# Kernel optimization log

Measured on AMD Instinct MI355X. Metric: run time of the kernel, lower is better.

## Reference

```python
import jax, jax.numpy as jnp
import numpy as np

H, KVH, D = 32, 8, 128
HID = H * D
OP = H * D + 2 * KVH * D
T = 2048
LAYER_IDX = 8
LAMBDA_INIT = float(0.8 - 0.6 * np.exp(-0.3 * LAYER_IDX))
EPS = 1e-5


def setup_inputs() -> dict:
    key = jax.random.key(0)
    ks = jax.random.split(key, 10)
    s = 0.02
    return {
        "hidden_states": jax.random.normal(ks[0], (T, HID), jnp.float32),
        "wqkv_w": jax.random.normal(ks[1], (OP, HID), jnp.float32) * s,
        "wqkv_b": jax.random.normal(ks[2], (OP,), jnp.float32) * s,
        "lambda_q1": jax.random.normal(ks[3], (D,), jnp.float32) * 0.1,
        "lambda_k1": jax.random.normal(ks[4], (D,), jnp.float32) * 0.1,
        "lambda_q2": jax.random.normal(ks[5], (D,), jnp.float32) * 0.1,
        "lambda_k2": jax.random.normal(ks[6], (D,), jnp.float32) * 0.1,
        "subln_w": jnp.ones((2 * D,), jnp.float32),
        "out_w": jax.random.normal(ks[7], (HID, HID), jnp.float32) * s,
        "out_b": jax.random.normal(ks[8], (HID,), jnp.float32) * s,
    }


def reference(hidden_states, wqkv_w, wqkv_b, lambda_q1, lambda_k1,
              lambda_q2, lambda_k2, subln_w, out_w, out_b):
    t = hidden_states.shape[0]
    scale = D ** -0.5

    qkv = hidden_states @ wqkv_w.T + wqkv_b                     # [T, OP]
    q, k, v = jnp.split(qkv, [H * D, H * D + KVH * D], axis=-1)

    # pair-wise head split: consecutive heads form (pair, component) groups
    q = q.reshape(t, H // 2, 2, D)                              # [T, Hp, 2, D]
    k = k.reshape(t, KVH // 2, 2, D)                            # [T, KVHp, 2, D]
    v = v.reshape(t, KVH // 2, 2 * D)                           # [T, KVHp, 2D]

    rep = H // KVH  # GQA: query pair p -> kv pair p // rep
    k = jnp.repeat(k, rep, axis=1)                              # [T, Hp, 2, D]
    v = jnp.repeat(v, rep, axis=1)                              # [T, Hp, 2D]

    lam = (jnp.exp(jnp.dot(lambda_q1, lambda_k1))
           - jnp.exp(jnp.dot(lambda_q2, lambda_k2)) + LAMBDA_INIT)

    causal = jnp.tril(jnp.ones((t, t), bool))
    scores = jnp.einsum('qhcd,khcd->hcqk', q, k) * scale        # [Hp, 2, T, T]
    scores = jnp.where(causal, scores, -jnp.inf)
    probs = jax.nn.softmax(scores, axis=-1)
    attn = probs[:, 0] - lam * probs[:, 1]                      # [Hp, T, T]

    out = jnp.einsum('hqk,khd->qhd', attn, v)                   # [T, Hp, 2D]

    # per-head RMSNorm over 2D, scaled by (1 - lambda_init)
    rms = jax.lax.rsqrt(jnp.mean(out * out, axis=-1, keepdims=True) + EPS)
    out = out * rms * subln_w * (1.0 - LAMBDA_INIT)

    out = out.reshape(t, H * D)
    return out @ out_w.T + out_b
```

## Files before the change

### kernel.cpp

```cpp
#include <hip/hip_runtime.h>

#define TTOK 2048
#define HIDN 4096
#define OPD  6144
#define DH   128
#define VD   256
#define KOFF 4096
#define VOFF 5120

typedef short  s16x8 __attribute__((ext_vector_type(8)));
typedef unsigned short u16x8 __attribute__((ext_vector_type(8)));
typedef float  fx4   __attribute__((ext_vector_type(4)));

constexpr float LAM_INIT = 0.7455692280263534f;
constexpr float OML      = 1.0f - LAM_INIT;
constexpr float QKSCALE  = 0.08838834764831845f;
constexpr float RESCALE_THR = 8.0f;

__device__ __forceinline__ unsigned short f2bf(float f) {
  unsigned int u = __builtin_bit_cast(unsigned int, f);
  u += 0x7fffu + ((u >> 16) & 1u);
  return (unsigned short)(u >> 16);
}

__device__ __forceinline__ void g2l16(const void* gsrc, void* ldst) {
  __builtin_amdgcn_global_load_lds(
      (const __attribute__((address_space(1))) unsigned int*)gsrc,
      (__attribute__((address_space(3))) unsigned int*)ldst, 16, 0, 0);
}

__global__ __launch_bounds__(256)
void cvt3(const float* __restrict__ s0, unsigned short* __restrict__ d0, int nb0,
          const float* __restrict__ s1, unsigned short* __restrict__ d1, int nb1,
          const float* __restrict__ s2, unsigned short* __restrict__ d2)
{
  const int b = blockIdx.x;
  const float* s; unsigned short* d; int base;
  if (b < nb0)            { s = s0; d = d0; base = b << 11; }
  else if (b < nb0 + nb1) { s = s1; d = d1; base = (b - nb0) << 11; }
  else                    { s = s2; d = d2; base = (b - nb0 - nb1) << 11; }
  const int i = base + (int)threadIdx.x * 8;
  const float4 a0 = *(const float4*)(s + i);
  const float4 a1 = *(const float4*)(s + i + 4);
  u16x8 v;
  v[0]=f2bf(a0.x); v[1]=f2bf(a0.y); v[2]=f2bf(a0.z); v[3]=f2bf(a0.w);
  v[4]=f2bf(a1.x); v[5]=f2bf(a1.y); v[6]=f2bf(a1.z); v[7]=f2bf(a1.w);
  *(u16x8*)(d + i) = v;
}

template<int MW, bool QKVOUT, bool OUTBF16>
__global__ __launch_bounds__(512, 2)
void gemm_8ph(const unsigned short* __restrict__ A, const unsigned short* __restrict__ B,
              const float* __restrict__ bias, void* __restrict__ Cp,
              unsigned short* __restrict__ ctt, int K, int lda, int ldb, int ldc)
{
  constexpr int BM  = MW * 32;
  constexpr int ALD = BM / 64;
  __shared__ __align__(16) unsigned short As[2][BM * 64];
  __shared__ __align__(16) unsigned short Bs[2][256 * 64];

  const int tid  = threadIdx.x;
  const int lane = tid & 63, wid = tid >> 6;
  const int wm = wid >> 2, wn = wid & 3;
  const int m0 = blockIdx.y * BM, n0 = blockIdx.x * 256;
  const int l15 = lane & 15, lg = lane >> 4;

  const int srow = tid >> 3;
  const int scol = ((tid & 7) ^ ((tid >> 3) & 7)) << 3;
  const int rsw = (l15 & 7) << 3;
  const int ck0 = (lg * 8) ^ rsw;
  const int ck1 = (32 + lg * 8) ^ rsw;
  const int arow = wm * (MW * 16) + l15;
  const int brow = wn * 64 + l15;

  auto stageA = [&](int kt, int buf) {
    #pragma unroll
    for (int it = 0; it < ALD; ++it)
      g2l16(A + (size_t)(m0 + it * 64 + srow) * lda + kt + scol,
            &As[buf][(it * 512 + tid) * 8]);
  };
  auto stageB = [&](int kt, int buf, int h) {
    #pragma unroll
    for (int it = h * 2; it < h * 2 + 2; ++it)
      g2l16(B + (size_t)(n0 + it * 64 + srow) * ldb + kt + scol,
            &Bs[buf][(it * 512 + tid) * 8]);
  };

  fx4 acc[MW][4] = {};

  const int nk = K >> 6;
  stageA(0, 0); stageB(0, 0, 0); stageB(0, 0, 1);
  asm volatile("s_waitcnt vmcnt(0)" ::: "memory");
  __builtin_amdgcn_s_barrier();

  for (int t = 0; t < nk; ++t) {
    const unsigned short* as = As[t & 1];
    const unsigned short* bs = Bs[t & 1];
    const int kt1 = (t + 1) << 6;
    const int nb  = (t + 1) & 1;
    const bool pre = (t + 1) < nk;
    s16x8 af[MW], bf[4];

    #pragma unroll
    for (int mi = 0; mi < MW; ++mi)
      af[mi] = *(const s16x8*)&as[(arow + mi * 16) * 64 + ck0];
    bf[0] = *(const s16x8*)&bs[(brow +  0) * 64 + ck0];
    bf[1] = *(const s16x8*)&bs[(brow + 16) * 64 + ck0];
    if (pre) { stageA(kt1, nb); stageB(kt1, nb, 0); }
    __builtin_amdgcn_s_barrier();
    asm volatile("s_waitcnt lgkmcnt(0)" ::: "memory");
    __builtin_amdgcn_sched_barrier(0);
    __builtin_amdgcn_s_setprio(1);
    #pragma unroll
    for (int mi = 0; mi < MW; ++mi) {
      acc[mi][0] = __builtin_amdgcn_mfma_f32_16x16x32_bf16(af[mi], bf[0], acc[mi][0], 0, 0, 0);
      acc[mi][1] = __builtin_amdgcn_mfma_f32_16x16x32_bf16(af[mi], bf[1], acc[mi][1], 0, 0, 0);
    }
    __builtin_amdgcn_s_setprio(0);
    __builtin_amdgcn_s_barrier();

    bf[2] = *(const s16x8*)&bs[(brow + 32) * 64 + ck0];
    bf[3] = *(const s16x8*)&bs[(brow + 48) * 64 + ck0];
    if (pre) stageB(kt1, nb, 1);
    __builtin_amdgcn_s_barrier();
    asm volatile("s_waitcnt lgkmcnt(0)" ::: "memory");
    __builtin_amdgcn_sched_barrier(0);
    __builtin_amdgcn_s_setprio(1);
    #pragma unroll
    for (int mi = 0; mi < MW; ++mi) {
      acc[mi][2] = __builtin_amdgcn_mfma_f32_16x16x32_bf16(af[mi], bf[2], acc[mi][2], 0, 0, 0);
      acc[mi][3] = __builtin_amdgcn_mfma_f32_16x16x32_bf16(af[mi], bf[3], acc[mi][3], 0, 0, 0);
    }
    __builtin_amdgcn_s_setprio(0);
    __builtin_amdgcn_s_barrier();

    #pragma unroll
    for (int mi = 0; mi < MW; ++mi)
      af[mi] = *(const s16x8*)&as[(arow + mi * 16) * 64 + ck1];
    bf[0] = *(const s16x8*)&bs[(brow +  0) * 64 + ck1];
    bf[1] = *(const s16x8*)&bs[(brow + 16) * 64 + ck1];
    __builtin_amdgcn_s_barrier();
    asm volatile("s_waitcnt lgkmcnt(0)" ::: "memory");
    __builtin_amdgcn_sched_barrier(0);
    __builtin_amdgcn_s_setprio(1);
    #pragma unroll
    for (int mi = 0; mi < MW; ++mi) {
      acc[mi][0] = __builtin_amdgcn_mfma_f32_16x16x32_bf16(af[mi], bf[0], acc[mi][0], 0, 0, 0);
      acc[mi][1] = __builtin_amdgcn_mfma_f32_16x16x32_bf16(af[mi], bf[1], acc[mi][1], 0, 0, 0);
    }
    __builtin_amdgcn_s_setprio(0);
    __builtin_amdgcn_s_barrier();

    bf[2] = *(const s16x8*)&bs[(brow + 32) * 64 + ck1];
    bf[3] = *(const s16x8*)&bs[(brow + 48) * 64 + ck1];
    __builtin_amdgcn_s_barrier();
    asm volatile("s_waitcnt lgkmcnt(0)" ::: "memory");
    __builtin_amdgcn_sched_barrier(0);
    __builtin_amdgcn_s_setprio(1);
    #pragma unroll
    for (int mi = 0; mi < MW; ++mi) {
      acc[mi][2] = __builtin_amdgcn_mfma_f32_16x16x32_bf16(af[mi], bf[2], acc[mi][2], 0, 0, 0);
      acc[mi][3] = __builtin_amdgcn_mfma_f32_16x16x32_bf16(af[mi], bf[3], acc[mi][3], 0, 0, 0);
    }
    __builtin_amdgcn_s_setprio(0);
    if (pre) asm volatile("s_waitcnt vmcnt(0)" ::: "memory");
    __builtin_amdgcn_s_barrier();
  }

  const int r0 = m0 + wm * (MW * 16);
  const int c0 = n0 + wn * 64;
  if (QKVOUT && n0 >= VOFF) {
    #pragma unroll
    for (int mi = 0; mi < MW; ++mi)
      #pragma unroll
      for (int ni = 0; ni < 4; ++ni) {
        const int col = c0 + ni * 16 + l15;
        const float bv = bias[col];
        const fx4 a = acc[mi][ni];
        ushort4 pk;
        pk.x = f2bf(a[0] + bv); pk.y = f2bf(a[1] + bv);
        pk.z = f2bf(a[2] + bv); pk.w = f2bf(a[3] + bv);
        const int d   = col - VOFF;
        const int kvp = d >> 8, dw = d & 255;
        const int row0 = r0 + mi * 16 + lg * 4;
        const int kt2 = row0 >> 5, kk = row0 & 31;
        const int kc = kk >> 3, k8 = kk & 7;
        *(ushort4*)&ctt[(size_t)kvp * 1048576 + (size_t)kt2 * 16384 + 8192
                        + kc * 2048 + dw * 8 + k8] = pk;
      }
  } else if (QKVOUT && n0 >= KOFF) {
    #pragma unroll
    for (int mi = 0; mi < MW; ++mi)
      #pragma unroll
      for (int ni = 0; ni < 4; ++ni) {
        const int ccol = c0 + ni * 16 + l15 - KOFF;
        const float bv = bias[c0 + ni * 16 + l15];
        const int kvp = ccol >> 8, cw = ccol & 255;
        const int cc = cw >> 3, cb = cw & 7;
        const fx4 a = acc[mi][ni];
        #pragma unroll
        for (int jj = 0; jj < 4; ++jj) {
          const int row2 = r0 + mi * 16 + lg * 4 + jj;
          const int kt2 = row2 >> 5, kk = row2 & 31;
          ctt[(size_t)kvp * 1048576 + (size_t)kt2 * 16384 + cc * 256 + kk * 8 + cb]
              = f2bf(a[jj] + bv);
        }
      }
  } else {
    #pragma unroll
    for (int mi = 0; mi < MW; ++mi)
      #pragma unroll
      for (int ni = 0; ni < 4; ++ni) {
        const int col = c0 + ni * 16 + l15;
        const float bv = bias[col];
        const fx4 a = acc[mi][ni];
        #pragma unroll
        for (int jj = 0; jj < 4; ++jj) {
          const int row2 = r0 + mi * 16 + lg * 4 + jj;
          const float v = a[jj] + bv;
          if (OUTBF16) ((unsigned short*)Cp)[(size_t)row2 * ldc + col] = f2bf(v);
          else         ((float*)Cp)[(size_t)row2 * ldc + col] = v;
        }
      }
  }
}

__global__ __launch_bounds__(256, 2)
void attn_kernel(const unsigned short* __restrict__ qq,
                 const unsigned short* __restrict__ ctt,
                 const float* __restrict__ lq1, const float* __restrict__ lk1,
                 const float* __restrict__ lq2, const float* __restrict__ lk2,
                 const float* __restrict__ subln,
                 unsigned short* __restrict__ attn_out)
{
  __shared__ __align__(16) unsigned short Sb[2][16384];
  __shared__ __align__(16) unsigned short Pl[4][2][640];
  const int tid = threadIdx.x;
  const int lane = tid & 63, w = tid >> 6;
  const int l15 = lane & 15, lg = lane >> 4;

  const int bid = blockIdx.x;
  const int g = bid & 7, s = bid >> 3;
  const int kvp  = g >> 1;
  const int pair = kvp * 4 + (s & 3);
  const int qb   = 31 - ((s >> 2) << 1) - (g & 1);
  const int q0b  = qb * 64;
  const int q0w  = q0b + w * 16;
  const int nt   = 2 * qb + 2;

  const unsigned short* cbase = ctt + (size_t)kvp * 1048576;

  auto stage = [&](int kt, int buf) {
    const unsigned short* src = cbase + (size_t)kt * 16384;
    const int off = w * 512 + lane * 8;
    #pragma unroll
    for (int i = 0; i < 8; ++i) {
      const int o = i * 2048 + off;
      g2l16(src + o, &Sb[buf][o]);
    }
  };

  stage(0, 0);

  float a1 = lq1[lane] * lk1[lane] + lq1[lane + 64] * lk1[lane + 64];
  float a2 = lq2[lane] * lk2[lane] + lq2[lane + 64] * lk2[lane + 64];
  #pragma unroll
  for (int sft = 1; sft < 64; sft <<= 1) { a1 += __shfl_xor(a1, sft); a2 += __shfl_xor(a2, sft); }
  const float lam = __expf(a1) - __expf(a2) + LAM_INIT;

  s16x8 qf0[4], qf1[4];
  {
    const unsigned short* qbp = qq + (size_t)(q0w + l15) * HIDN + pair * VD + lg * 8;
    #pragma unroll
    for (int kf = 0; kf < 4; ++kf) {
      qf0[kf] = *(const s16x8*)(qbp + kf * 32);
      qf1[kf] = *(const s16x8*)(qbp + DH + kf * 32);
    }
  }

  float mrun0 = -1e30f, mrun1 = -1e30f;
  float lrun0 = 0.f, lrun1 = 0.f;
  fx4 oacc0[16] = {}, oacc1[16] = {};
  unsigned short* pl0 = &Pl[w][0][0];
  unsigned short* pl1 = &Pl[w][1][0];
  const int q = q0w + l15;
  const int qmax = q0w + 15;

  for (int t = 0; t < nt; ++t) {
    __syncthreads();
    if (t + 1 < nt) stage(t + 1, (t + 1) & 1);
    const int kb = t * 32;
    if (kb > qmax) continue;
    const unsigned short* Kl = Sb[t & 1];
    const unsigned short* Vl = Sb[t & 1] + 8192;

    fx4 s00 = {0,0,0,0}, s01 = {0,0,0,0}, s10 = {0,0,0,0}, s11 = {0,0,0,0};
    #pragma unroll
    for (int kf = 0; kf < 4; ++kf) {
      const int cc0 = kf * 4 + lg;
      const int cc1 = 16 + kf * 4 + lg;
      const s16x8 k00 = *(const s16x8*)&Kl[cc0 * 256 + l15 * 8];
      const s16x8 k01 = *(const s16x8*)&Kl[cc0 * 256 + (16 + l15) * 8];
      const s16x8 k10 = *(const s16x8*)&Kl[cc1 * 256 + l15 * 8];
      const s16x8 k11 = *(const s16x8*)&Kl[cc1 * 256 + (16 + l15) * 8];
      s00 = __builtin_amdgcn_mfma_f32_16x16x32_bf16(k00, qf0[kf], s00, 0, 0, 0);
      s01 = __builtin_amdgcn_mfma_f32_16x16x32_bf16(k01, qf0[kf], s01, 0, 0, 0);
      s10 = __builtin_amdgcn_mfma_f32_16x16x32_bf16(k10, qf1[kf], s10, 0, 0, 0);
      s11 = __builtin_amdgcn_mfma_f32_16x16x32_bf16(k11, qf1[kf], s11, 0, 0, 0);
    }

    float v0[8], v1[8];
    #pragma unroll
    for (int j = 0; j < 4; ++j) {
      const int klo = kb + lg * 4 + j, khi = klo + 16;
      v0[j]     = (klo <= q) ? s00[j] * QKSCALE : -1e30f;
      v0[4 + j] = (khi <= q) ? s01[j] * QKSCALE : -1e30f;
      v1[j]     = (klo <= q) ? s10[j] * QKSCALE : -1e30f;
      v1[4 + j] = (khi <= q) ? s11[j] * QKSCALE : -1e30f;
    }
    float tm0 = fmaxf(fmaxf(fmaxf(v0[0],v0[1]),fmaxf(v0[2],v0[3])),
                      fmaxf(fmaxf(v0[4],v0[5]),fmaxf(v0[6],v0[7])));
    float tm1 = fmaxf(fmaxf(fmaxf(v1[0],v1[1]),fmaxf(v1[2],v1[3])),
                      fmaxf(fmaxf(v1[4],v1[5]),fmaxf(v1[6],v1[7])));
    tm0 = fmaxf(tm0, __shfl_xor(tm0, 16)); tm0 = fmaxf(tm0, __shfl_xor(tm0, 32));
    tm1 = fmaxf(tm1, __shfl_xor(tm1, 16)); tm1 = fmaxf(tm1, __shfl_xor(tm1, 32));

    const bool need = (tm0 > mrun0 + RESCALE_THR) || (tm1 > mrun1 + RESCALE_THR);
    if (__any(need)) {
      const float mn0 = fmaxf(mrun0, tm0), mn1 = fmaxf(mrun1, tm1);
      const float fac0 = __expf(mrun0 - mn0), fac1 = __expf(mrun1 - mn1);
      mrun0 = mn0; mrun1 = mn1;
      lrun0 *= fac0; lrun1 *= fac1;
      #pragma unroll
      for (int jj = 0; jj < 4; ++jj) {
        const float fr0 = __shfl(fac0, lg * 4 + jj);
        const float fr1 = __shfl(fac1, lg * 4 + jj);
        #pragma unroll
        for (int nf = 0; nf < 16; ++nf) { oacc0[nf][jj] *= fr0; oacc1[nf][jj] *= fr1; }
      }
    }

    {
      float ps0 = 0.f, ps1 = 0.f;
      ushort4 lo0, hi0, lo1, hi1;
      float p;
      p = __expf(v0[0]-mrun0); ps0 += p; lo0.x = f2bf(p);
      p = __expf(v0[1]-mrun0); ps0 += p; lo0.y = f2bf(p);
      p = __expf(v0[2]-mrun0); ps0 += p; lo0.z = f2bf(p);
      p = __expf(v0[3]-mrun0); ps0 += p; lo0.w = f2bf(p);
      p = __expf(v0[4]-mrun0); ps0 += p; hi0.x = f2bf(p);
      p = __expf(v0[5]-mrun0); ps0 += p; hi0.y = f2bf(p);
      p = __expf(v0[6]-mrun0); ps0 += p; hi0.z = f2bf(p);
      p = __expf(v0[7]-mrun0); ps0 += p; hi0.w = f2bf(p);
      p = __expf(v1[0]-mrun1); ps1 += p; lo1.x = f2bf(p);
      p = __expf(v1[1]-mrun1); ps1 += p; lo1.y = f2bf(p);
      p = __expf(v1[2]-mrun1); ps1 += p; lo1.z = f2bf(p);
      p = __expf(v1[3]-mrun1); ps1 += p; lo1.w = f2bf(p);
      p = __expf(v1[4]-mrun1); ps1 += p; hi1.x = f2bf(p);
      p = __expf(v1[5]-mrun1); ps1 += p; hi1.y = f2bf(p);
      p = __expf(v1[6]-mrun1); ps1 += p; hi1.z = f2bf(p);
      p = __expf(v1[7]-mrun1); ps1 += p; hi1.w = f2bf(p);
      lrun0 += ps0; lrun1 += ps1;
      *(ushort4*)&pl0[l15 * 40 + lg * 4]      = lo0;
      *(ushort4*)&pl0[l15 * 40 + 16 + lg * 4] = hi0;
      *(ushort4*)&pl1[l15 * 40 + lg * 4]      = lo1;
      *(ushort4*)&pl1[l15 * 40 + 16 + lg * 4] = hi1;
    }
    asm volatile("s_waitcnt lgkmcnt(0)" ::: "memory");
    __builtin_amdgcn_sched_barrier(0);

    const s16x8 pa0 = *(const s16x8*)&pl0[l15 * 40 + lg * 8];
    const s16x8 pa1 = *(const s16x8*)&pl1[l15 * 40 + lg * 8];
    #pragma unroll
    for (int nf = 0; nf < 16; ++nf) {
      const s16x8 vf = *(const s16x8*)&Vl[lg * 2048 + (nf * 16 + l15) * 8];
      oacc0[nf] = __builtin_amdgcn_mfma_f32_16x16x32_bf16(pa0, vf, oacc0[nf], 0, 0, 0);
      oacc1[nf] = __builtin_amdgcn_mfma_f32_16x16x32_bf16(pa1, vf, oacc1[nf], 0, 0, 0);
    }
  }

  lrun0 += __shfl_xor(lrun0, 16); lrun0 += __shfl_xor(lrun0, 32);
  lrun1 += __shfl_xor(lrun1, 16); lrun1 += __shfl_xor(lrun1, 32);

  float li0[4], li1[4];
  #pragma unroll
  for (int jj = 0; jj < 4; ++jj) {
    li0[jj] = 1.0f / __shfl(lrun0, lg * 4 + jj);
    li1[jj] = 1.0f / __shfl(lrun1, lg * 4 + jj);
  }

  float ss[4] = {0.f, 0.f, 0.f, 0.f};
  #pragma unroll
  for (int nf = 0; nf < 16; ++nf)
    #pragma unroll
    for (int jj = 0; jj < 4; ++jj) {
      const float o = oacc0[nf][jj] * li0[jj] - lam * oacc1[nf][jj] * li1[jj];
      oacc0[nf][jj] = o;
      ss[jj] += o * o;
    }
  #pragma unroll
  for (int jj = 0; jj < 4; ++jj) {
    ss[jj] += __shfl_xor(ss[jj], 1);
    ss[jj] += __shfl_xor(ss[jj], 2);
    ss[jj] += __shfl_xor(ss[jj], 4);
    ss[jj] += __shfl_xor(ss[jj], 8);
    ss[jj] = rsqrtf(ss[jj] * (1.0f / 256.0f) + 1e-5f) * OML;
  }
  #pragma unroll
  for (int nf = 0; nf < 16; ++nf) {
    const int dcol = nf * 16 + l15;
    const float sw = subln[dcol];
    #pragma unroll
    for (int jj = 0; jj < 4; ++jj) {
      const int t = q0w + lg * 4 + jj;
      attn_out[(size_t)t * HIDN + pair * VD + dcol] = f2bf(oacc0[nf][jj] * ss[jj] * sw);
    }
  }
}

extern "C" void kernel_launch(void* const* d_in, const int* in_sizes, int n_in,
                              void* d_out, int out_size, void* d_ws, size_t ws_size,
                              hipStream_t stream) {
  (void)in_sizes; (void)n_in; (void)out_size; (void)ws_size;
  const float* hs     = (const float*)d_in[0];
  const float* wqkv_w = (const float*)d_in[1];
  const float* wqkv_b = (const float*)d_in[2];
  const float* lq1    = (const float*)d_in[3];
  const float* lk1    = (const float*)d_in[4];
  const float* lq2    = (const float*)d_in[5];
  const float* lk2    = (const float*)d_in[6];
  const float* subln  = (const float*)d_in[7];
  const float* out_w  = (const float*)d_in[8];
  const float* out_b  = (const float*)d_in[9];

  unsigned short* qq       = (unsigned short*)d_ws;
  unsigned short* ctt      = qq + (size_t)TTOK * HIDN;
  unsigned short* attn_out = ctt + (size_t)4 * 1048576;
  unsigned short* hs_bf    = attn_out + (size_t)TTOK * HIDN;
  unsigned short* wqkv_bf  = hs_bf + (size_t)TTOK * HIDN;
  unsigned short* outw_bf  = wqkv_bf + (size_t)OPD * HIDN;

  const int nb0 = (TTOK * HIDN) >> 11;
  const int nb1 = (OPD * HIDN) >> 11;
  const int nb2 = (HIDN * HIDN) >> 11;
  cvt3<<<dim3(nb0 + nb1 + nb2), 256, 0, stream>>>(
      hs, hs_bf, nb0, wqkv_w, wqkv_bf, nb1, out_w, outw_bf);

  gemm_8ph<8, true, true><<<dim3(OPD / 256, TTOK / 256), 512, 0, stream>>>(
      hs_bf, wqkv_bf, wqkv_b, qq, ctt, HIDN, HIDN, HIDN, HIDN);

  attn_kernel<<<dim3(512), 256, 0, stream>>>(
      qq, ctt, lq1, lk1, lq2, lk2, subln, attn_out);

  gemm_8ph<4, false, false><<<dim3(HIDN / 256, TTOK / 128), 512, 0, stream>>>(
      attn_out, outw_bf, out_b, d_out, nullptr, HIDN, HIDN, HIDN, HIDN);
}
```

Before: 376.0 us.

## Split GEMM tiles into quadrant buffers with finer-grained prefetch waits

Shared-memory A and B tiles are split into two halves each, and each wave's outputs are interleaved across quadrants (rows strided by 32, columns by 64). The main loop walks four quadrant compute phases. Each phase issues the next tile's loads for one half and uses partial vmcnt waits instead of a full drain at the end of the iteration. This is meant to overlap global-to-LDS loads with MFMA work more evenly and to avoid the end-of-iteration stall. In exchange, the epilogue indexing and the hand-tuned vmcnt counts become more complex and correctness-sensitive.

```diff
diff --git a/kernel.cpp b/kernel.cpp
--- a/kernel.cpp
+++ b/kernel.cpp
@@ -54,10 +54,11 @@
               const float* __restrict__ bias, void* __restrict__ Cp,
               unsigned short* __restrict__ ctt, int K, int lda, int ldb, int ldc)
 {
-  constexpr int BM  = MW * 32;
-  constexpr int ALD = BM / 64;
-  __shared__ __align__(16) unsigned short As[2][BM * 64];
-  __shared__ __align__(16) unsigned short Bs[2][256 * 64];
+  constexpr int BM   = MW * 32;
+  constexpr int MH   = MW / 2;
+  constexpr int ALD2 = MW / 4;
+  __shared__ __align__(16) unsigned short As[2][2][(BM / 2) * 64];
+  __shared__ __align__(16) unsigned short Bs[2][2][128 * 64];
 
   const int tid  = threadIdx.x;
   const int lane = tid & 63, wid = tid >> 6;
@@ -70,111 +71,152 @@
   const int rsw = (l15 & 7) << 3;
   const int ck0 = (lg * 8) ^ rsw;
   const int ck1 = (32 + lg * 8) ^ rsw;
-  const int arow = wm * (MW * 16) + l15;
-  const int brow = wn * 64 + l15;
-
-  auto stageA = [&](int kt, int buf) {
-    #pragma unroll
-    for (int it = 0; it < ALD; ++it)
-      g2l16(A + (size_t)(m0 + it * 64 + srow) * lda + kt + scol,
-            &As[buf][(it * 512 + tid) * 8]);
+  const int arh = wm * 16 + l15;
+  const int brh = wn * 16 + l15;
+
+  auto stageAh = [&](int kt, int buf, int h) {
+    #pragma unroll
+    for (int i = 0; i < ALD2; ++i)
+      g2l16(A + (size_t)(m0 + h * (BM / 2) + i * 64 + srow) * lda + kt + scol,
+            &As[buf][h][(i * 512 + tid) * 8]);
   };
-  auto stageB = [&](int kt, int buf, int h) {
-    #pragma unroll
-    for (int it = h * 2; it < h * 2 + 2; ++it)
-      g2l16(B + (size_t)(n0 + it * 64 + srow) * ldb + kt + scol,
-            &Bs[buf][(it * 512 + tid) * 8]);
+  auto stageBh = [&](int kt, int buf, int h) {
+    #pragma unroll
+    for (int i = 0; i < 2; ++i)
+      g2l16(B + (size_t)(n0 + h * 128 + i * 64 + srow) * ldb + kt + scol,
+            &Bs[buf][h][(i * 512 + tid) * 8]);
   };
 
   fx4 acc[MW][4] = {};
 
   const int nk = K >> 6;
-  stageA(0, 0); stageB(0, 0, 0); stageB(0, 0, 1);
+  stageAh(0, 0, 0); stageBh(0, 0, 0); stageBh(0, 0, 1); stageAh(0, 0, 1);
   asm volatile("s_waitcnt vmcnt(0)" ::: "memory");
   __builtin_amdgcn_s_barrier();
 
   for (int t = 0; t < nk; ++t) {
-    const unsigned short* as = As[t & 1];
-    const unsigned short* bs = Bs[t & 1];
+    const int buf = t & 1, nb = buf ^ 1;
     const int kt1 = (t + 1) << 6;
-    const int nb  = (t + 1) & 1;
     const bool pre = (t + 1) < nk;
-    s16x8 af[MW], bf[4];
-
-    #pragma unroll
-    for (int mi = 0; mi < MW; ++mi)
-      af[mi] = *(const s16x8*)&as[(arow + mi * 16) * 64 + ck0];
-    bf[0] = *(const s16x8*)&bs[(brow +  0) * 64 + ck0];
-    bf[1] = *(const s16x8*)&bs[(brow + 16) * 64 + ck0];
-    if (pre) { stageA(kt1, nb); stageB(kt1, nb, 0); }
+    const unsigned short* A0 = &As[buf][0][0];
+    const unsigned short* A1 = &As[buf][1][0];
+    const unsigned short* B0 = &Bs[buf][0][0];
+    const unsigned short* B1 = &Bs[buf][1][0];
+    s16x8 af[MH][2], bf[2][2];
+
+    #pragma unroll
+    for (int m = 0; m < MH; ++m) {
+      af[m][0] = *(const s16x8*)&A0[(arh + m * 32) * 64 + ck0];
+      af[m][1] = *(const s16x8*)&A0[(arh + m * 32) * 64 + ck1];
+    }
+    #pragma unroll
+    for (int n = 0; n < 2; ++n) {
+      bf[n][0] = *(const s16x8*)&B0[(brh + n * 64) * 64 + ck0];
+      bf[n][1] = *(const s16x8*)&B0[(brh + n * 64) * 64 + ck1];
+    }
+    if (pre) {
+      stageAh(kt1, nb, 0);
+      if constexpr (MW == 8) asm volatile("s_waitcnt vmcnt(4)" ::: "memory");
+      else                   asm volatile("s_waitcnt vmcnt(2)" ::: "memory");
+    } else {
+      asm volatile("s_waitcnt vmcnt(0)" ::: "memory");
+    }
     __builtin_amdgcn_s_barrier();
     asm volatile("s_waitcnt lgkmcnt(0)" ::: "memory");
     __builtin_amdgcn_sched_barrier(0);
     __builtin_amdgcn_s_setprio(1);
     #pragma unroll
-    for (int mi = 0; mi < MW; ++mi) {
-      acc[mi][0] = __builtin_amdgcn_mfma_f32_16x16x32_bf16(af[mi], bf[0], acc[mi][0], 0, 0, 0);
-      acc[mi][1] = __builtin_amdgcn_mfma_f32_16x16x32_bf16(af[mi], bf[1], acc[mi][1], 0, 0, 0);
-    }
+    for (int m = 0; m < MH; ++m)
+      #pragma unroll
+      for (int n = 0; n < 2; ++n) {
+        acc[m][n] = __builtin_amdgcn_mfma_f32_16x16x32_bf16(af[m][0], bf[n][0], acc[m][n], 0, 0, 0);
+        acc[m][n] = __builtin_amdgcn_mfma_f32_16x16x32_bf16(af[m][1], bf[n][1], acc[m][n], 0, 0, 0);
+      }
     __builtin_amdgcn_s_setprio(0);
     __builtin_amdgcn_s_barrier();
 
-    bf[2] = *(const s16x8*)&bs[(brow + 32) * 64 + ck0];
-    bf[3] = *(const s16x8*)&bs[(brow + 48) * 64 + ck0];
-    if (pre) stageB(kt1, nb, 1);
+    #pragma unroll
+    for (int n = 0; n < 2; ++n) {
+      bf[n][0] = *(const s16x8*)&B1[(brh + n * 64) * 64 + ck0];
+      bf[n][1] = *(const s16x8*)&B1[(brh + n * 64) * 64 + ck1];
+    }
+    if (pre) {
+      stageBh(kt1, nb, 0);
+      if constexpr (MW == 8) asm volatile("s_waitcnt vmcnt(4)" ::: "memory");
+      else                   asm volatile("s_waitcnt vmcnt(3)" ::: "memory");
+    }
     __builtin_amdgcn_s_barrier();
     asm volatile("s_waitcnt lgkmcnt(0)" ::: "memory");
     __builtin_amdgcn_sched_barrier(0);
     __builtin_amdgcn_s_setprio(1);
     #pragma unroll
-    for (int mi = 0; mi < MW; ++mi) {
-      acc[mi][2] = __builtin_amdgcn_mfma_f32_16x16x32_bf16(af[mi], bf[2], acc[mi][2], 0, 0, 0);
-      acc[mi][3] = __builtin_amdgcn_mfma_f32_16x16x32_bf16(af[mi], bf[3], acc[mi][3], 0, 0, 0);
-    }
+    for (int m = 0; m < MH; ++m)
+      #pragma unroll
+      for (int n = 0; n < 2; ++n) {
+        acc[m][2 + n] = __builtin_amdgcn_mfma_f32_16x16x32_bf16(af[m][0], bf[n][0], acc[m][2 + n], 0, 0, 0);
+        acc[m][2 + n] = __builtin_amdgcn_mfma_f32_16x16x32_bf16(af[m][1], bf[n][1], acc[m][2 + n], 0, 0, 0);
+      }
     __builtin_amdgcn_s_setprio(0);
     __builtin_amdgcn_s_barrier();
 
     #pragma unroll
-    for (int mi = 0; mi < MW; ++mi)
-      af[mi] = *(const s16x8*)&as[(arow + mi * 16) * 64 + ck1];
-    bf[0] = *(const s16x8*)&bs[(brow +  0) * 64 + ck1];
-    bf[1] = *(const s16x8*)&bs[(brow + 16) * 64 + ck1];
+    for (int m = 0; m < MH; ++m) {
+      af[m][0] = *(const s16x8*)&A1[(arh + m * 32) * 64 + ck0];
+      af[m][1] = *(const s16x8*)&A1[(arh + m * 32) * 64 + ck1];
+    }
+    #pragma unroll
+    for (int n = 0; n < 2; ++n) {
+      bf[n][0] = *(const s16x8*)&B0[(brh + n * 64) * 64 + ck0];
+      bf[n][1] = *(const s16x8*)&B0[(brh + n * 64) * 64 + ck1];
+    }
+    if (pre) stageBh(kt1, nb, 1);
     __builtin_amdgcn_s_barrier();
     asm volatile("s_waitcnt lgkmcnt(0)" ::: "memory");
     __builtin_amdgcn_sched_barrier(0);
     __builtin_amdgcn_s_setprio(1);
     #pragma unroll
-    for (int mi = 0; mi < MW; ++mi) {
-      acc[mi][0] = __builtin_amdgcn_mfma_f32_16x16x32_bf16(af[mi], bf[0], acc[mi][0], 0, 0, 0);
-      acc[mi][1] = __builtin_amdgcn_mfma_f32_16x16x32_bf16(af[mi], bf[1], acc[mi][1], 0, 0, 0);
-    }
+    for (int m = 0; m < MH; ++m)
+      #pragma unroll
+      for (int n = 0; n < 2; ++n) {
+        acc[MH + m][n] = __builtin_amdgcn_mfma_f32_16x16x32_bf16(af[m][0], bf[n][0], acc[MH + m][n], 0, 0, 0);
+        acc[MH + m][n] = __builtin_amdgcn_mfma_f32_16x16x32_bf16(af[m][1], bf[n][1], acc[MH + m][n], 0, 0, 0);
+      }
     __builtin_amdgcn_s_setprio(0);
     __builtin_amdgcn_s_barrier();
 
-    bf[2] = *(const s16x8*)&bs[(brow + 32) * 64 + ck1];
-    bf[3] = *(const s16x8*)&bs[(brow + 48) * 64 + ck1];
+    #pragma unroll
+    for (int n = 0; n < 2; ++n) {
+      bf[n][0] = *(const s16x8*)&B1[(brh + n * 64) * 64 + ck0];
+      bf[n][1] = *(const s16x8*)&B1[(brh + n * 64) * 64 + ck1];
+    }
+    if (pre) {
+      stageAh(kt1, nb, 1);
+      if constexpr (MW == 8) asm volatile("s_waitcnt vmcnt(4)" ::: "memory");
+      else                   asm volatile("s_waitcnt vmcnt(3)" ::: "memory");
+    }
     __builtin_amdgcn_s_barrier();
     asm volatile("s_waitcnt lgkmcnt(0)" ::: "memory");
     __builtin_amdgcn_sched_barrier(0);
     __builtin_amdgcn_s_setprio(1);
     #pragma unroll
-    for (int mi = 0; mi < MW; ++mi) {
-      acc[mi][2] = __builtin_amdgcn_mfma_f32_16x16x32_bf16(af[mi], bf[2], acc[mi][2], 0, 0, 0);
-      acc[mi][3] = __builtin_amdgcn_mfma_f32_16x16x32_bf16(af[mi], bf[3], acc[mi][3], 0, 0, 0);
-    }
+    for (int m = 0; m < MH; ++m)
+      #pragma unroll
+      for (int n = 0; n < 2; ++n) {
+        acc[MH + m][2 + n] = __builtin_amdgcn_mfma_f32_16x16x32_bf16(af[m][0], bf[n][0], acc[MH + m][2 + n], 0, 0, 0);
+        acc[MH + m][2 + n] = __builtin_amdgcn_mfma_f32_16x16x32_bf16(af[m][1], bf[n][1], acc[MH + m][2 + n], 0, 0, 0);
+      }
     __builtin_amdgcn_s_setprio(0);
-    if (pre) asm volatile("s_waitcnt vmcnt(0)" ::: "memory");
-    __builtin_amdgcn_s_barrier();
-  }
-
-  const int r0 = m0 + wm * (MW * 16);
-  const int c0 = n0 + wn * 64;
+    __builtin_amdgcn_s_barrier();
+  }
+
+  const int rb = m0 + wm * 16;
+  const int cb = n0 + wn * 16;
   if (QKVOUT && n0 >= VOFF) {
     #pragma unroll
     for (int mi = 0; mi < MW; ++mi)
       #pragma unroll
       for (int ni = 0; ni < 4; ++ni) {
-        const int col = c0 + ni * 16 + l15;
+        const int col = cb + ni * 64 + l15;
         const float bv = bias[col];
         const fx4 a = acc[mi][ni];
         ushort4 pk;
@@ -182,7 +224,7 @@
         pk.z = f2bf(a[2] + bv); pk.w = f2bf(a[3] + bv);
         const int d   = col - VOFF;
         const int kvp = d >> 8, dw = d & 255;
-        const int row0 = r0 + mi * 16 + lg * 4;
+        const int row0 = rb + mi * 32 + lg * 4;
         const int kt2 = row0 >> 5, kk = row0 & 31;
         const int kc = kk >> 3, k8 = kk & 7;
         *(ushort4*)&ctt[(size_t)kvp * 1048576 + (size_t)kt2 * 16384 + 8192
@@ -193,16 +235,17 @@
     for (int mi = 0; mi < MW; ++mi)
       #pragma unroll
       for (int ni = 0; ni < 4; ++ni) {
-        const int ccol = c0 + ni * 16 + l15 - KOFF;
-        const float bv = bias[c0 + ni * 16 + l15];
+        const int col = cb + ni * 64 + l15;
+        const int ccol = col - KOFF;
+        const float bv = bias[col];
         const int kvp = ccol >> 8, cw = ccol & 255;
-        const int cc = cw >> 3, cb = cw & 7;
+        const int cc = cw >> 3, cbt = cw & 7;
         const fx4 a = acc[mi][ni];
         #pragma unroll
         for (int jj = 0; jj < 4; ++jj) {
-          const int row2 = r0 + mi * 16 + lg * 4 + jj;
+          const int row2 = rb + mi * 32 + lg * 4 + jj;
           const int kt2 = row2 >> 5, kk = row2 & 31;
-          ctt[(size_t)kvp * 1048576 + (size_t)kt2 * 16384 + cc * 256 + kk * 8 + cb]
+          ctt[(size_t)kvp * 1048576 + (size_t)kt2 * 16384 + cc * 256 + kk * 8 + cbt]
               = f2bf(a[jj] + bv);
         }
       }
@@ -211,12 +254,12 @@
     for (int mi = 0; mi < MW; ++mi)
       #pragma unroll
       for (int ni = 0; ni < 4; ++ni) {
-        const int col = c0 + ni * 16 + l15;
+        const int col = cb + ni * 64 + l15;
         const float bv = bias[col];
         const fx4 a = acc[mi][ni];
         #pragma unroll
         for (int jj = 0; jj < 4; ++jj) {
-          const int row2 = r0 + mi * 16 + lg * 4 + jj;
+          const int row2 = rb + mi * 32 + lg * 4 + jj;
           const float v = a[jj] + bv;
           if (OUTBF16) ((unsigned short*)Cp)[(size_t)row2 * ldc + col] = f2bf(v);
           else         ((float*)Cp)[(size_t)row2 * ldc + col] = v;
```

Result: faster. 367.8 us (-2.2%).
